# Performance work log

Hardware: AMD Instinct MI355X
Metric: run time of the kernel (lower is better)

## Reference

```python
import jax, jax.numpy as jnp
import numpy as np

B, S, D = 16, 2048, 128
NEG = -1e9


def setup_inputs() -> dict:
    key = jax.random.key(0)
    kq, kk, kv = jax.random.split(key, 3)
    queries = jax.random.normal(kq, (B, S, D), dtype=jnp.float32)
    keys = jax.random.normal(kk, (B, S, D), dtype=jnp.float32)
    values = jax.random.normal(kv, (B, S, D), dtype=jnp.float32)
    # causal additive mask: 0 on/below diagonal, -1e9 above
    causal = jnp.triu(jnp.ones((S, S), dtype=jnp.float32), k=1) * NEG
    return {"queries": queries, "keys": keys, "values": values, "mask": causal}


def reference(queries, keys, values, mask):
    d = queries.shape[-1]
    scale = 1.0 / jnp.sqrt(jnp.asarray(d, dtype=queries.dtype))
    # scores: [b, q, k]
    scores = jnp.einsum("bqd,bkd->bqk", queries, keys) * scale
    scores = scores + mask  # broadcast [S,S] over batch
    weights = jax.nn.softmax(scores, axis=-1)
    # dropout p=0.0 in eval mode -> identity
    return jnp.einsum("bqk,bkd->bqd", weights, values)
```

## Files before the change

### kernel.cpp

```cpp
#include <hip/hip_runtime.h>
#include <hip/hip_bf16.h>
#include <cstdint>

#define SS   2048
#define DD   128
#define KBLK 64
#define NKT  32
#define TILE_BYTES 16384
#define NBLK 640

#define WS_K   ((size_t)0)
#define WS_V   ((size_t)16 * NKT * TILE_BYTES)
#define WS_PO  ((size_t)16 * NKT * TILE_BYTES * 2)
#define WS_ML  (WS_PO + (size_t)NBLK * 128 * 128 * 2)
#define WS_NEED (WS_ML + (size_t)NBLK * 128 * 4)

typedef __attribute__((ext_vector_type(8)))  short short8;
typedef __attribute__((ext_vector_type(16))) float f32x16;
typedef __attribute__((ext_vector_type(4)))  float f32x4;

__device__ __forceinline__ unsigned short f2bf(float x) {
  return __builtin_bit_cast(unsigned short, (__bf16)x);
}
__device__ __forceinline__ float bfbits2f(unsigned int lo16shifted) {
  return __builtin_bit_cast(float, lo16shifted);
}

__device__ __constant__ unsigned char FULLI[28]   = {3,4,5,6,7,7,8,8,9,9,10,10,11,11,11,12,12,12,13,13,13,14,14,14,15,15,15,15};
__device__ __constant__ unsigned char FULLBASE[16]= {0,0,0,0,1,2,3,4,6,8,10,12,15,18,21,24};
__device__ __constant__ unsigned char FULLCNT[16] = {0,0,0,1,1,1,1,2,2,2,2,3,3,3,3,4};
__device__ __constant__ signed   char SMALLIDX[16]= {0,1,2,-1,3,4,5,-1,6,7,8,-1,9,10,11,-1};
__device__ __constant__ unsigned char SMALLI[12]  = {0,1,2,4,5,6,8,9,10,12,13,14};
__device__ __constant__ unsigned char SMALLC[12]  = {0,0,0,1,1,1,2,2,2,3,3,3};
__device__ __constant__ unsigned char SMALLN[12]  = {2,4,6,2,4,6,2,4,6,2,4,6};

__global__ __launch_bounds__(256) void prepack_kv4(
    const float* __restrict__ K, const float* __restrict__ V, char* __restrict__ ws)
{
  __shared__ float vf[64][129];
  const int b = blockIdx.x, t = blockIdx.y;
  const int tid = threadIdx.x;
  const float* Kt = K + ((size_t)b * SS + t * KBLK) * DD;
  const float* Vt = V + ((size_t)b * SS + t * KBLK) * DD;
  char* Kd = ws + WS_K + ((size_t)(b * NKT + t)) * TILE_BYTES;
  char* Vd = ws + WS_V + ((size_t)(b * NKT + t)) * TILE_BYTES;

  #pragma unroll
  for (int u = 0; u < 4; ++u) {
    int row = u * 16 + (tid >> 4);
    int col = 8 * (tid & 15);
    const float4* sp = reinterpret_cast<const float4*>(Kt + (size_t)row * DD + col);
    float4 x = sp[0], y = sp[1];
    short8 w;
    w[0] = f2bf(x.x); w[1] = f2bf(x.y); w[2] = f2bf(x.z); w[3] = f2bf(x.w);
    w[4] = f2bf(y.x); w[5] = f2bf(y.y); w[6] = f2bf(y.z); w[7] = f2bf(y.w);
    int off = (row * 256 + col * 2) ^ ((row & 7) << 4);
    *reinterpret_cast<short8*>(Kd + off) = w;
  }
  #pragma unroll
  for (int u = 0; u < 4; ++u) {
    int row = u * 16 + (tid >> 4);
    int col = 8 * (tid & 15);
    const float4* sp = reinterpret_cast<const float4*>(Vt + (size_t)row * DD + col);
    float4 x = sp[0], y = sp[1];
    vf[row][col+0]=x.x; vf[row][col+1]=x.y; vf[row][col+2]=x.z; vf[row][col+3]=x.w;
    vf[row][col+4]=y.x; vf[row][col+5]=y.y; vf[row][col+6]=y.z; vf[row][col+7]=y.w;
  }
  __syncthreads();
  #pragma unroll
  for (int q = 0; q < 4; ++q) {
    int idx = q * 256 + tid;
    int d = idx >> 3, y8 = idx & 7;
    short8 w;
    #pragma unroll
    for (int j = 0; j < 8; ++j) {
      int a = ((y8 >> 2) << 5) | (((y8 >> 1) & 1) << 4) | ((j >> 2) << 3) | (j & 3) | ((y8 & 1) << 2);
      w[j] = f2bf(vf[a][d]);
    }
    int off = ((d << 7) + (y8 << 4)) ^ ((d & 7) << 4);
    *reinterpret_cast<short8*>(Vd + off) = w;
  }
}

__device__ __forceinline__ void stage_tile(const char* Ksrc, const char* Vsrc,
                                           char* Kl, char* Vl, int wid, int lane)
{
  #pragma unroll
  for (int i = 0; i < 4; ++i) {
    int off = wid * 4096 + i * 1024;
    __builtin_amdgcn_global_load_lds(
        (const __attribute__((address_space(1))) unsigned int*)(Ksrc + off + lane * 16),
        (__attribute__((address_space(3))) unsigned int*)(Kl + off), 16, 0, 0);
  }
  #pragma unroll
  for (int i = 0; i < 4; ++i) {
    int off = wid * 4096 + i * 1024;
    __builtin_amdgcn_global_load_lds(
        (const __attribute__((address_space(1))) unsigned int*)(Vsrc + off + lane * 16),
        (__attribute__((address_space(3))) unsigned int*)(Vl + off), 16, 0, 0);
  }
}

__global__ __launch_bounds__(256, 2) void sdpa_v4(
    const float* __restrict__ Q, const char* __restrict__ ws,
    unsigned short* __restrict__ partO, float* __restrict__ partML)
{
  __shared__ __align__(16) char smem[2 * 32768];

  const int y = blockIdx.x;
  int b, i, c, ntile;
  if (y < 448) { int k = y >> 4; b = y & 15; i = FULLI[k]; c = k - FULLBASE[i]; ntile = 8; }
  else         { int z = y - 448; int k = z >> 4; b = z & 15; i = SMALLI[k]; c = SMALLC[k]; ntile = SMALLN[k]; }

  const int tid  = threadIdx.x;
  const int lane = tid & 63;
  const int wid  = tid >> 6;
  const int l31  = lane & 31;
  const int h    = lane >> 5;

  const float* Qb  = Q + (size_t)b * SS * DD;
  const char*  Kws = ws + WS_K + ((size_t)(b * NKT + 8 * c)) * TILE_BYTES;
  const char*  Vws = ws + WS_V + ((size_t)(b * NKT + 8 * c)) * TILE_BYTES;

  const float qscale = 0.08838834764831845f * 1.4426950408889634f;

  const int qg = 128 * i + wid * 32 + l31;

  short8 qf[8];
  {
    const float* qrow = Qb + (size_t)qg * DD;
    #pragma unroll
    for (int s = 0; s < 8; ++s) {
      const float4* p = reinterpret_cast<const float4*>(qrow + s * 16 + h * 8);
      float4 x = p[0], z = p[1];
      short8 w;
      w[0] = f2bf(x.x * qscale); w[1] = f2bf(x.y * qscale);
      w[2] = f2bf(x.z * qscale); w[3] = f2bf(x.w * qscale);
      w[4] = f2bf(z.x * qscale); w[5] = f2bf(z.y * qscale);
      w[6] = f2bf(z.z * qscale); w[7] = f2bf(z.w * qscale);
      qf[s] = w;
    }
  }

  f32x16 o[4];
  #pragma unroll
  for (int dg = 0; dg < 4; ++dg)
    #pragma unroll
    for (int r = 0; r < 16; ++r) o[dg][r] = 0.f;
  float lsum = 0.f;

  int cur = 0;
  stage_tile(Kws, Vws, smem, smem + 16384, wid, lane);
  __syncthreads();

  for (int t = 0; t < ntile; ++t) {
    if (t + 1 < ntile) {
      char* nb = smem + (cur ^ 1) * 32768;
      stage_tile(Kws + (size_t)(t + 1) * TILE_BYTES, Vws + (size_t)(t + 1) * TILE_BYTES,
                 nb, nb + 16384, wid, lane);
    }
    const char* Kl = smem + cur * 32768;
    const char* Vl = Kl + 16384;
    const bool domask = (8 * c + t) >= 2 * i;

    short8 pf[4];
    float psum = 0.f;

    #pragma unroll
    for (int g = 0; g < 2; ++g) {
      f32x16 acc;
      #pragma unroll
      for (int r = 0; r < 16; ++r) acc[r] = 0.f;
      const int key = g * 32 + l31;
      const int kbase = key * 256 + h * 16;
      const int kswz = (key & 7) << 4;
      __builtin_amdgcn_s_setprio(1);
      #pragma unroll
      for (int s = 0; s < 8; ++s) {
        short8 kf = *reinterpret_cast<const short8*>(Kl + ((kbase + s * 32) ^ kswz));
        acc = __builtin_amdgcn_mfma_f32_32x32x16_bf16(kf, qf[s], acc, 0, 0, 0);
      }
      __builtin_amdgcn_s_setprio(0);

      if (domask) {
        const int kb = (8 * c + t) * 64 + g * 32 + 4 * h;
        #pragma unroll
        for (int r = 0; r < 16; ++r) {
          int keyg = kb + (r & 3) + 8 * (r >> 2);
          if (keyg > qg) acc[r] = -1e30f;
        }
      }

      float pg[16];
      #pragma unroll
      for (int r = 0; r < 16; ++r) pg[r] = exp2f(acc[r]);
      float s0 = ((pg[0]+pg[1])+(pg[2]+pg[3])) + ((pg[4]+pg[5])+(pg[6]+pg[7]));
      float s1 = ((pg[8]+pg[9])+(pg[10]+pg[11])) + ((pg[12]+pg[13])+(pg[14]+pg[15]));
      psum += s0 + s1;

      short8 w0, w1;
      #pragma unroll
      for (int j = 0; j < 8; ++j) { w0[j] = f2bf(pg[j]); w1[j] = f2bf(pg[8 + j]); }
      pf[2 * g]     = w0;
      pf[2 * g + 1] = w1;
    }
    lsum += psum;

    __builtin_amdgcn_s_setprio(1);
    #pragma unroll
    for (int dg = 0; dg < 4; ++dg) {
      const int d = dg * 32 + l31;
      const int vbase = d * 128 + h * 16;
      const int vswz = (d & 7) << 4;
      #pragma unroll
      for (int s4 = 0; s4 < 4; ++s4) {
        short8 vf8 = *reinterpret_cast<const short8*>(Vl + ((vbase + s4 * 32) ^ vswz));
        o[dg] = __builtin_amdgcn_mfma_f32_32x32x16_bf16(vf8, pf[s4], o[dg], 0, 0, 0);
      }
    }
    __builtin_amdgcn_s_setprio(0);

    if (t + 1 < ntile) {
      __syncthreads();
      cur ^= 1;
    }
  }

  lsum += __shfl_xor(lsum, 32);

  unsigned short* po = partO + (size_t)y * (128 * 128) + (size_t)(wid * 32 + l31) * 128;
  #pragma unroll
  for (int dg = 0; dg < 4; ++dg)
    #pragma unroll
    for (int rq = 0; rq < 4; ++rq) {
      int d0 = dg * 32 + 8 * rq + 4 * h;
      ushort4 u;
      u.x = f2bf(o[dg][4 * rq + 0]);
      u.y = f2bf(o[dg][4 * rq + 1]);
      u.z = f2bf(o[dg][4 * rq + 2]);
      u.w = f2bf(o[dg][4 * rq + 3]);
      *reinterpret_cast<ushort4*>(po + d0) = u;
    }
  if (h == 0) partML[y * 128 + wid * 32 + l31] = lsum;
}

__global__ __launch_bounds__(256) void merge_v4(
    const unsigned short* __restrict__ partO, const float* __restrict__ partML,
    float* __restrict__ O)
{
  const int b = blockIdx.x & 15, i = blockIdx.x >> 4;
  const int tid = threadIdx.x;
  const int r = tid >> 1, c0 = (tid & 1) * 64;

  float acc[64];
  #pragma unroll
  for (int u = 0; u < 64; ++u) acc[u] = 0.f;
  float ltot = 0.f;

  const int nf = FULLCNT[i];
  const int si = SMALLIDX[i];
  const int nch = nf + (si >= 0 ? 1 : 0);

  for (int c = 0; c < nch; ++c) {
    int slot = (c < nf) ? ((FULLBASE[i] + c) * 16 + b) : (448 + si * 16 + b);
    ltot += partML[slot * 128 + r];
    const uint4* po = reinterpret_cast<const uint4*>(
        partO + (size_t)slot * (128 * 128) + (size_t)r * 128 + c0);
    #pragma unroll
    for (int u = 0; u < 8; ++u) {
      uint4 v = po[u];
      acc[u*8+0] += bfbits2f(v.x << 16); acc[u*8+1] += bfbits2f(v.x & 0xffff0000u);
      acc[u*8+2] += bfbits2f(v.y << 16); acc[u*8+3] += bfbits2f(v.y & 0xffff0000u);
      acc[u*8+4] += bfbits2f(v.z << 16); acc[u*8+5] += bfbits2f(v.z & 0xffff0000u);
      acc[u*8+6] += bfbits2f(v.w << 16); acc[u*8+7] += bfbits2f(v.w & 0xffff0000u);
    }
  }
  float inv = 1.0f / ltot;
  float* orow = O + ((size_t)b * SS + 128 * i + r) * DD + c0;
  #pragma unroll
  for (int u = 0; u < 16; ++u) {
    float4 w;
    w.x = acc[4*u+0] * inv; w.y = acc[4*u+1] * inv;
    w.z = acc[4*u+2] * inv; w.w = acc[4*u+3] * inv;
    reinterpret_cast<float4*>(orow)[u] = w;
  }
}

__device__ __forceinline__ int sigma_col(int a) {
  return (a & 35) | ((a & 12) << 1) | ((a & 16) >> 2);
}

__global__ __launch_bounds__(256) void sdpa_naive(
    const float* __restrict__ Q, const float* __restrict__ K,
    const float* __restrict__ V, float* __restrict__ O)
{
  __shared__ __align__(16) char smem[64 * 128 * 2 * 2];
  char* Klds  = smem;
  char* Vtlds = smem + 64 * 128 * 2;

  const int b   = blockIdx.x;
  const int qb  = (int)gridDim.y - 1 - (int)blockIdx.y;
  const int q0  = qb * 64;
  const int tid = threadIdx.x;
  const int lane = tid & 63;
  const int wid  = tid >> 6;
  const int l15  = lane & 15;
  const int hi   = lane >> 4;

  const float* Qb = Q + (size_t)b * SS * DD;
  const float* Kb = K + (size_t)b * SS * DD;
  const float* Vb = V + (size_t)b * SS * DD;
  float*       Ob = O + (size_t)b * SS * DD;
  const float scale = 0.08838834764831845f;

  short8 qf[4];
  {
    const float* qrow = Qb + (size_t)(q0 + wid * 16 + l15) * DD;
    #pragma unroll
    for (int cc = 0; cc < 4; ++cc) {
      const float4* p = reinterpret_cast<const float4*>(qrow + 32 * cc + 8 * hi);
      float4 x = p[0], yv = p[1];
      short8 w;
      w[0]=f2bf(x.x*scale); w[1]=f2bf(x.y*scale); w[2]=f2bf(x.z*scale); w[3]=f2bf(x.w*scale);
      w[4]=f2bf(yv.x*scale); w[5]=f2bf(yv.y*scale); w[6]=f2bf(yv.z*scale); w[7]=f2bf(yv.w*scale);
      qf[cc] = w;
    }
  }

  f32x4 o[8];
  #pragma unroll
  for (int nt = 0; nt < 8; ++nt) o[nt] = (f32x4){0.f,0.f,0.f,0.f};
  float m = -INFINITY, lsum = 0.f;

  const int ntile = qb + 1;
  for (int t = 0; t < ntile; ++t) {
    const int kv0 = t * 64;
    if (t) __syncthreads();
    #pragma unroll
    for (int u = 0; u < 4; ++u) {
      int row = u * 16 + (tid >> 4);
      int col = 8 * (tid & 15);
      const float4* sp = reinterpret_cast<const float4*>(Kb + (size_t)(kv0 + row) * DD + col);
      float4 x = sp[0], yv = sp[1];
      short8 w;
      w[0]=f2bf(x.x); w[1]=f2bf(x.y); w[2]=f2bf(x.z); w[3]=f2bf(x.w);
      w[4]=f2bf(yv.x); w[5]=f2bf(yv.y); w[6]=f2bf(yv.z); w[7]=f2bf(yv.w);
      int off = (row * 256 + col * 2) ^ ((row & 7) << 4);
      *reinterpret_cast<short8*>(Klds + off) = w;
    }
    #pragma unroll
    for (int u = 0; u < 4; ++u) {
      int row = u * 16 + (tid >> 4);
      int col = 8 * (tid & 15);
      const float4* sp = reinterpret_cast<const float4*>(Vb + (size_t)(kv0 + row) * DD + col);
      float4 x = sp[0], yv = sp[1];
      int sc = sigma_col(row);
      float vals[8] = {x.x, x.y, x.z, x.w, yv.x, yv.y, yv.z, yv.w};
      #pragma unroll
      for (int j = 0; j < 8; ++j) {
        int d = col + j;
        int off = ((d << 7) + (sc << 1)) ^ ((((d >> 3) ^ d) & 7) << 4);
        *reinterpret_cast<unsigned short*>(Vtlds + off) = f2bf(vals[j]);
      }
    }
    __syncthreads();

    f32x4 sacc[4];
    #pragma unroll
    for (int g = 0; g < 4; ++g) {
      f32x4 acc = {0.f,0.f,0.f,0.f};
      #pragma unroll
      for (int cc = 0; cc < 4; ++cc) {
        int row = g * 16 + l15;
        int off = (row * 256 + (32 * cc + 8 * hi) * 2) ^ ((row & 7) << 4);
        short8 kf = *reinterpret_cast<const short8*>(Klds + off);
        acc = __builtin_amdgcn_mfma_f32_16x16x32_bf16(kf, qf[cc], acc, 0, 0, 0);
      }
      sacc[g] = acc;
    }
    if (t == ntile - 1) {
      const int q = q0 + wid * 16 + l15;
      #pragma unroll
      for (int g = 0; g < 4; ++g)
        #pragma unroll
        for (int ii = 0; ii < 4; ++ii) {
          int key = kv0 + g * 16 + 4 * hi + ii;
          if (key > q) sacc[g][ii] = -1e30f;
        }
    }
    float tmax = -INFINITY;
    #pragma unroll
    for (int g = 0; g < 4; ++g)
      #pragma unroll
      for (int ii = 0; ii < 4; ++ii) tmax = fmaxf(tmax, sacc[g][ii]);
    tmax = fmaxf(tmax, __shfl_xor(tmax, 16));
    tmax = fmaxf(tmax, __shfl_xor(tmax, 32));
    float mnew = fmaxf(m, tmax);
    float corr = __expf(m - mnew);
    m = mnew;
    float p[4][4]; float psum = 0.f;
    #pragma unroll
    for (int g = 0; g < 4; ++g)
      #pragma unroll
      for (int ii = 0; ii < 4; ++ii) {
        float pv = __expf(sacc[g][ii] - mnew);
        p[g][ii] = pv; psum += pv;
      }
    psum += __shfl_xor(psum, 16);
    psum += __shfl_xor(psum, 32);
    lsum = lsum * corr + psum;
    float corrO[4];
    #pragma unroll
    for (int ii = 0; ii < 4; ++ii) corrO[ii] = __shfl(corr, 4 * hi + ii);
    #pragma unroll
    for (int nt = 0; nt < 8; ++nt)
      #pragma unroll
      for (int ii = 0; ii < 4; ++ii) o[nt][ii] *= corrO[ii];
    short8 pfr[2];
    #pragma unroll
    for (int ks = 0; ks < 2; ++ks) {
      short8 w;
      #pragma unroll
      for (int ii = 0; ii < 4; ++ii) { w[ii] = f2bf(p[2*ks][ii]); w[4+ii] = f2bf(p[2*ks+1][ii]); }
      pfr[ks] = w;
    }
    #pragma unroll
    for (int ks = 0; ks < 2; ++ks)
      #pragma unroll
      for (int nt = 0; nt < 8; ++nt) {
        int d = nt * 16 + l15;
        int off = ((d << 7) + (ks * 32 + 8 * hi) * 2) ^ ((((d >> 3) ^ d) & 7) << 4);
        short8 vvf = *reinterpret_cast<const short8*>(Vtlds + off);
        o[nt] = __builtin_amdgcn_mfma_f32_16x16x32_bf16(pfr[ks], vvf, o[nt], 0, 0, 0);
      }
  }
  float rl = 1.0f / lsum;
  float rlO[4];
  #pragma unroll
  for (int ii = 0; ii < 4; ++ii) rlO[ii] = __shfl(rl, 4 * hi + ii);
  const int qrow = q0 + wid * 16;
  #pragma unroll
  for (int nt = 0; nt < 8; ++nt)
    #pragma unroll
    for (int ii = 0; ii < 4; ++ii)
      Ob[(size_t)(qrow + 4 * hi + ii) * DD + nt * 16 + l15] = o[nt][ii] * rlO[ii];
}

extern "C" void kernel_launch(void* const* d_in, const int* in_sizes, int n_in,
                              void* d_out, int out_size, void* d_ws, size_t ws_size,
                              hipStream_t stream) {
  const float* Q = (const float*)d_in[0];
  const float* K = (const float*)d_in[1];
  const float* V = (const float*)d_in[2];
  float* O = (float*)d_out;
  char* ws = (char*)d_ws;

  if (ws_size >= WS_NEED) {
    unsigned short* partO = (unsigned short*)(ws + WS_PO);
    float* partML = (float*)(ws + WS_ML);
    prepack_kv4<<<dim3(16, NKT), 256, 0, stream>>>(K, V, ws);
    sdpa_v4<<<dim3(NBLK), 256, 0, stream>>>(Q, ws, partO, partML);
    merge_v4<<<dim3(256), 256, 0, stream>>>(partO, partML, O);
  } else {
    sdpa_naive<<<dim3(16, 32), 256, 0, stream>>>(Q, K, V, O);
  }
}
```

Before: 64.46 us.

## Single-buffer K/V LDS to raise occupancy and split merge across more blocks

The attention kernel drops the double-buffered K/V LDS staging, halving shared memory per block, and raises the launch-bounds occupancy hint from 2 to 4 blocks per CU. Tile prefetch no longer overlaps compute: each tile is loaded between two barriers, so latency hiding now relies on other resident blocks. The merge kernel is split 4x finer (1024 blocks, 16 columns per thread instead of 64), which cuts its register use and spreads the reduction over more CUs. The tighter register budget could cause spills in the MFMA accumulators.

```diff
diff --git a/kernel.cpp b/kernel.cpp
--- a/kernel.cpp
+++ b/kernel.cpp
@@ -34,7 +34,7 @@
 __device__ __constant__ unsigned char SMALLC[12]  = {0,0,0,1,1,1,2,2,2,3,3,3};
 __device__ __constant__ unsigned char SMALLN[12]  = {2,4,6,2,4,6,2,4,6,2,4,6};
 
-__global__ __launch_bounds__(256) void prepack_kv4(
+__global__ __launch_bounds__(256) void prepack_kv5(
     const float* __restrict__ K, const float* __restrict__ V, char* __restrict__ ws)
 {
   __shared__ float vf[64][129];
@@ -101,11 +101,11 @@
   }
 }
 
-__global__ __launch_bounds__(256, 2) void sdpa_v4(
+__global__ __launch_bounds__(256, 4) void sdpa_v5(
     const float* __restrict__ Q, const char* __restrict__ ws,
     unsigned short* __restrict__ partO, float* __restrict__ partML)
 {
-  __shared__ __align__(16) char smem[2 * 32768];
+  __shared__ __align__(16) char smem[32768];
 
   const int y = blockIdx.x;
   int b, i, c, ntile;
@@ -149,18 +149,12 @@
     for (int r = 0; r < 16; ++r) o[dg][r] = 0.f;
   float lsum = 0.f;
 
-  int cur = 0;
   stage_tile(Kws, Vws, smem, smem + 16384, wid, lane);
   __syncthreads();
 
   for (int t = 0; t < ntile; ++t) {
-    if (t + 1 < ntile) {
-      char* nb = smem + (cur ^ 1) * 32768;
-      stage_tile(Kws + (size_t)(t + 1) * TILE_BYTES, Vws + (size_t)(t + 1) * TILE_BYTES,
-                 nb, nb + 16384, wid, lane);
-    }
-    const char* Kl = smem + cur * 32768;
-    const char* Vl = Kl + 16384;
+    const char* Kl = smem;
+    const char* Vl = smem + 16384;
     const bool domask = (8 * c + t) >= 2 * i;
 
     short8 pf[4];
@@ -222,7 +216,9 @@
 
     if (t + 1 < ntile) {
       __syncthreads();
-      cur ^= 1;
+      stage_tile(Kws + (size_t)(t + 1) * TILE_BYTES, Vws + (size_t)(t + 1) * TILE_BYTES,
+                 smem, smem + 16384, wid, lane);
+      __syncthreads();
     }
   }
 
@@ -244,17 +240,19 @@
   if (h == 0) partML[y * 128 + wid * 32 + l31] = lsum;
 }
 
-__global__ __launch_bounds__(256) void merge_v4(
+__global__ __launch_bounds__(256) void merge_v5(
     const unsigned short* __restrict__ partO, const float* __restrict__ partML,
     float* __restrict__ O)
 {
-  const int b = blockIdx.x & 15, i = blockIdx.x >> 4;
+  const int x = blockIdx.x;
+  const int b = x & 15, i = (x >> 4) & 15, rg = x >> 8;
   const int tid = threadIdx.x;
-  const int r = tid >> 1, c0 = (tid & 1) * 64;
-
-  float acc[64];
-  #pragma unroll
-  for (int u = 0; u < 64; ++u) acc[u] = 0.f;
+  const int row = rg * 32 + (tid >> 3);
+  const int c0  = (tid & 7) * 16;
+
+  float acc[16];
+  #pragma unroll
+  for (int u = 0; u < 16; ++u) acc[u] = 0.f;
   float ltot = 0.f;
 
   const int nf = FULLCNT[i];
@@ -263,11 +261,11 @@
 
   for (int c = 0; c < nch; ++c) {
     int slot = (c < nf) ? ((FULLBASE[i] + c) * 16 + b) : (448 + si * 16 + b);
-    ltot += partML[slot * 128 + r];
+    ltot += partML[slot * 128 + row];
     const uint4* po = reinterpret_cast<const uint4*>(
-        partO + (size_t)slot * (128 * 128) + (size_t)r * 128 + c0);
-    #pragma unroll
-    for (int u = 0; u < 8; ++u) {
+        partO + (size_t)slot * (128 * 128) + (size_t)row * 128 + c0);
+    #pragma unroll
+    for (int u = 0; u < 2; ++u) {
       uint4 v = po[u];
       acc[u*8+0] += bfbits2f(v.x << 16); acc[u*8+1] += bfbits2f(v.x & 0xffff0000u);
       acc[u*8+2] += bfbits2f(v.y << 16); acc[u*8+3] += bfbits2f(v.y & 0xffff0000u);
@@ -276,9 +274,9 @@
     }
   }
   float inv = 1.0f / ltot;
-  float* orow = O + ((size_t)b * SS + 128 * i + r) * DD + c0;
-  #pragma unroll
-  for (int u = 0; u < 16; ++u) {
+  float* orow = O + ((size_t)b * SS + 128 * i + row) * DD + c0;
+  #pragma unroll
+  for (int u = 0; u < 4; ++u) {
     float4 w;
     w.x = acc[4*u+0] * inv; w.y = acc[4*u+1] * inv;
     w.z = acc[4*u+2] * inv; w.w = acc[4*u+3] * inv;
@@ -458,9 +456,9 @@
   if (ws_size >= WS_NEED) {
     unsigned short* partO = (unsigned short*)(ws + WS_PO);
     float* partML = (float*)(ws + WS_ML);
-    prepack_kv4<<<dim3(16, NKT), 256, 0, stream>>>(K, V, ws);
-    sdpa_v4<<<dim3(NBLK), 256, 0, stream>>>(Q, ws, partO, partML);
-    merge_v4<<<dim3(256), 256, 0, stream>>>(partO, partML, O);
+    prepack_kv5<<<dim3(16, NKT), 256, 0, stream>>>(K, V, ws);
+    sdpa_v5<<<dim3(NBLK), 256, 0, stream>>>(Q, ws, partO, partML);
+    merge_v5<<<dim3(1024), 256, 0, stream>>>(partO, partML, O);
   } else {
     sdpa_naive<<<dim3(16, 32), 256, 0, stream>>>(Q, K, V, O);
   }
```

Result: slower. 135.5 us (+110.2%).
